# Performance work log

Measured on AMD Instinct MI355X. Metric: run time of the kernel, lower is better.

Reference implementation:

```python
import jax, jax.numpy as jnp
import numpy as np

ITERATION = 10

def setup_inputs() -> dict:
    key = jax.random.key(0)
    k1, k2, k3 = jax.random.split(key, 3)
    a_inter = jax.random.normal(k1, (8, 64, 64, 32, 32), dtype=jnp.float32)
    logits = jax.random.normal(k2, (8, 64), dtype=jnp.float32)
    W = jax.random.normal(k3, (1, 64, 64), dtype=jnp.float32)
    return {"a_inter": a_inter, "logits": logits, "W": W}


def reference(a_inter, logits, W):
    N = W.shape[1]  # num_nodes
    B = a_inter.shape[0]
    # feats: [B, N, C*H*W]
    feats = a_inter[:, :, :N, :, :].reshape(B, N, -1)
    # expand logits [B, N] -> [B, N, N] (unsqueeze(1).expand in torch)
    logits0 = jnp.broadcast_to(logits[:, None, :], (B, N, N))

    feats_norm = jnp.linalg.norm(feats, ord=2, axis=2, keepdims=True)  # [B, N, 1]
    pairwise_norm = feats_norm @ jnp.swapaxes(feats_norm, 1, 2)        # [B, N, N]
    pairwise_dot = feats @ jnp.swapaxes(feats, 1, 2)                   # [B, N, N]
    pairwise_sim = pairwise_dot / (pairwise_norm + 1e-6)
    W_sym = (W + jnp.swapaxes(W, 1, 2)) / 2.0
    pairwise_potential = pairwise_sim * W_sym                          # [B, N, N]

    unary_potential = logits0

    def body(i, l):
        probs = jnp.swapaxes(jax.nn.sigmoid(l), 1, 2)  # [B, N, N]
        # probs*pp - (1-probs)*pp == (2*probs - 1)*pp
        pp_E = jnp.sum((2.0 * probs - 1.0) * pairwise_potential, axis=2, keepdims=True)
        return unary_potential + pp_E

    logits_out = jax.lax.fori_loop(0, ITERATION, body, logits0)
    return logits_out.mean(axis=1)  # [B, N]
```

## Files before the change

kernel.cpp:

```cpp
#include <hip/hip_runtime.h>
#include <math.h>

#define BATCH 8
#define NN 64
#define DD 65536
#define CH 256
#define KC (DD / CH)
#define KSTEPS (KC / 32)

typedef float  floatx4 __attribute__((ext_vector_type(4)));
typedef __bf16 bf16x8  __attribute__((ext_vector_type(8)));

static __device__ __forceinline__ bf16x8 cvt8(float4 lo, float4 hi) {
    const unsigned sel = 0x07060302u;
    union { unsigned u[4]; bf16x8 v; } r;
    r.u[0] = __builtin_amdgcn_perm(__float_as_uint(lo.y), __float_as_uint(lo.x), sel);
    r.u[1] = __builtin_amdgcn_perm(__float_as_uint(lo.w), __float_as_uint(lo.z), sel);
    r.u[2] = __builtin_amdgcn_perm(__float_as_uint(hi.y), __float_as_uint(hi.x), sel);
    r.u[3] = __builtin_amdgcn_perm(__float_as_uint(hi.w), __float_as_uint(hi.z), sel);
    return r.v;
}

__global__ __launch_bounds__(256, 4) void gram_partial_kernel(const float* __restrict__ a,
                                                              float* __restrict__ part) {
    const int bid = blockIdx.x;
    const int b = bid >> 8;
    const int c = bid & (CH - 1);

    const int tid  = threadIdx.x;
    const int w    = tid >> 6;
    const int lane = tid & 63;
    const int m    = lane & 15;
    const int q    = lane >> 4;

    const float* base = a + (size_t)b * NN * DD + (size_t)c * KC
                          + (size_t)m * DD + q * 8;
    const float* p0 = base + (size_t)((w ^ 0) * 16) * DD;
    const float* p1 = base + (size_t)((w ^ 1) * 16) * DD;
    const float* p2 = base + (size_t)((w ^ 2) * 16) * DD;
    const float* p3 = base + (size_t)((w ^ 3) * 16) * DD;

    floatx4 acc[4];
    #pragma unroll
    for (int i = 0; i < 4; ++i) acc[i] = (floatx4)0.0f;

    float4 A0, A1, A2, A3, A4, A5, A6, A7;
    float4 B0, B1, B2, B3, B4, B5, B6, B7;

#define LOADSET(R0,R1,R2,R3,R4,R5,R6,R7, o)                      \
    R0 = *(const float4*)(p0 + (o));  R1 = *(const float4*)(p0 + (o) + 4); \
    R2 = *(const float4*)(p1 + (o));  R3 = *(const float4*)(p1 + (o) + 4); \
    R4 = *(const float4*)(p2 + (o));  R5 = *(const float4*)(p2 + (o) + 4); \
    R6 = *(const float4*)(p3 + (o));  R7 = *(const float4*)(p3 + (o) + 4);

#define MFMASET(R0,R1,R2,R3,R4,R5,R6,R7)                         \
    {                                                            \
        bf16x8 f0 = cvt8(R0, R1);                                \
        bf16x8 f1 = cvt8(R2, R3);                                \
        bf16x8 f2 = cvt8(R4, R5);                                \
        bf16x8 f3 = cvt8(R6, R7);                                \
        acc[0] = __builtin_amdgcn_mfma_f32_16x16x32_bf16(f0, f0, acc[0], 0, 0, 0); \
        acc[1] = __builtin_amdgcn_mfma_f32_16x16x32_bf16(f0, f1, acc[1], 0, 0, 0); \
        acc[2] = __builtin_amdgcn_mfma_f32_16x16x32_bf16(f0, f2, acc[2], 0, 0, 0); \
        acc[3] = __builtin_amdgcn_mfma_f32_16x16x32_bf16(f0, f3, acc[3], 0, 0, 0); \
    }

    LOADSET(A0,A1,A2,A3,A4,A5,A6,A7, 0)
    #pragma unroll
    for (int s = 0; s < KSTEPS; s += 2) {
        if (s + 1 < KSTEPS) { LOADSET(B0,B1,B2,B3,B4,B5,B6,B7, (s + 1) * 32) }
        MFMASET(A0,A1,A2,A3,A4,A5,A6,A7)
        if (s + 2 < KSTEPS) { LOADSET(A0,A1,A2,A3,A4,A5,A6,A7, (s + 2) * 32) }
        if (s + 1 < KSTEPS) { MFMASET(B0,B1,B2,B3,B4,B5,B6,B7) }
    }
#undef LOADSET
#undef MFMASET

    float* pg = part + (size_t)bid * (NN * NN);
    #pragma unroll
    for (int i = 0; i < 4; ++i) {
        const int t = w ^ i;
        float* tp = pg + (w * 4 + t) * 256 + m;
        #pragma unroll
        for (int r = 0; r < 4; ++r)
            tp[(q * 4 + r) * 16] = acc[i][r];
    }
}

__global__ __launch_bounds__(128) void gram_reduce_kernel(const float* __restrict__ part,
                                                          float* __restrict__ gram) {
    const int gid = blockIdx.x * 128 + threadIdx.x;
    const int b   = gid >> 12;
    const int idx = gid & 4095;
    const int i   = idx >> 6;
    const int j   = idx & 63;
    const int off = ((i >> 4) * 4 + (j >> 4)) * 256 + (i & 15) * 16 + (j & 15);
    const float* p = part + (size_t)b * CH * (NN * NN) + off;

    float s0 = 0.f, s1 = 0.f, s2 = 0.f, s3 = 0.f;
    #pragma unroll 4
    for (int c = 0; c < CH; c += 4) {
        s0 += p[(size_t)(c + 0) * (NN * NN)];
        s1 += p[(size_t)(c + 1) * (NN * NN)];
        s2 += p[(size_t)(c + 2) * (NN * NN)];
        s3 += p[(size_t)(c + 3) * (NN * NN)];
    }
    gram[gid] = (s0 + s1) + (s2 + s3);
}

__global__ __launch_bounds__(256) void crf_kernel(const float* __restrict__ gram,
                                                  const float* __restrict__ logits,
                                                  const float* __restrict__ Wm,
                                                  float* __restrict__ out) {
    __shared__ float pp[NN][NN + 1];
    __shared__ float E[NN];
    __shared__ float nrm[NN];
    __shared__ float part[4 * NN];

    const int b  = blockIdx.x;
    const int tid = threadIdx.x;
    const int i  = tid & 63;
    const int jq = tid >> 6;
    const float* g = gram + b * NN * NN;

    if (jq == 0) nrm[i] = sqrtf(g[i * NN + i]);
    E[i] = 0.0f;
    __syncthreads();

    const float ni = nrm[i];
    for (int jj = 0; jj < 16; ++jj) {
        int j = jq * 16 + jj;
        float wsym = 0.5f * (Wm[i * NN + j] + Wm[j * NN + i]);
        pp[i][j] = g[i * NN + j] / (ni * nrm[j] + 1e-6f) * wsym;
    }
    const float li = logits[b * NN + i];
    __syncthreads();

    for (int it = 0; it < 10; ++it) {
        float acc = 0.0f;
        for (int jj = 0; jj < 16; ++jj) {
            int j = jq * 16 + jj;
            float t = li + E[j];
            float s = 1.0f / (1.0f + expf(-t));
            acc = fmaf(2.0f * s - 1.0f, pp[i][j], acc);
        }
        part[jq * NN + i] = acc;
        __syncthreads();
        if (jq == 0)
            E[i] = part[i] + part[NN + i] + part[2 * NN + i] + part[3 * NN + i];
        __syncthreads();
    }

    if (tid < 64) {
        float s = E[tid];
        for (int off = 32; off > 0; off >>= 1) s += __shfl_down(s, off);
        float meanE = __shfl(s, 0) * (1.0f / 64.0f);
        out[b * NN + tid] = logits[b * NN + tid] + meanE;
    }
}

extern "C" void kernel_launch(void* const* d_in, const int* in_sizes, int n_in,
                              void* d_out, int out_size, void* d_ws, size_t ws_size,
                              hipStream_t stream) {
    const float* a      = (const float*)d_in[0];
    const float* logits = (const float*)d_in[1];
    const float* Wm     = (const float*)d_in[2];
    float* out  = (float*)d_out;

    float* part = (float*)d_ws;
    float* gram = part + (size_t)BATCH * CH * NN * NN;

    gram_partial_kernel<<<BATCH * CH, 256, 0, stream>>>(a, part);
    gram_reduce_kernel<<<(BATCH * NN * NN) / 128, 128, 0, stream>>>(part, gram);
    crf_kernel<<<BATCH, 256, 0, stream>>>(gram, logits, Wm, out);
}
```

Before: 251.8 us.

## Split K across waves with full 64x64 Gram per wave and LDS reduction

Each wave now computes the full 64x64 Gram tile over its own K quarter, instead of each wave computing a 16-row stripe over a shared K range. The four wave partials are summed through shared memory inside the block. The grid shrinks from 2048 to 512 blocks, so there are 4x fewer partial tiles to write and reduce. In exchange each wave holds 16 accumulator tiles, which raises register pressure and lowers occupancy. The launch bound of 4 blocks per CU is also dropped.

```diff
diff --git a/kernel.cpp b/kernel.cpp
--- a/kernel.cpp
+++ b/kernel.cpp
@@ -4,9 +4,11 @@
 #define BATCH 8
 #define NN 64
 #define DD 65536
-#define CH 256
-#define KC (DD / CH)
-#define KSTEPS (KC / 32)
+#define BPB 64
+#define NBLK (BATCH * BPB)
+#define KC (DD / BPB)
+#define KW (KC / 4)
+#define KSTEPS (KW / 32)
 
 typedef float  floatx4 __attribute__((ext_vector_type(4)));
 typedef __bf16 bf16x8  __attribute__((ext_vector_type(8)));
@@ -21,11 +23,13 @@
     return r.v;
 }
 
-__global__ __launch_bounds__(256, 4) void gram_partial_kernel(const float* __restrict__ a,
-                                                              float* __restrict__ part) {
+__global__ __launch_bounds__(256) void gram_partial_kernel(const float* __restrict__ a,
+                                                           float* __restrict__ part) {
+    __shared__ __align__(16) float red[3][16][64][4];
+
     const int bid = blockIdx.x;
-    const int b = bid >> 8;
-    const int c = bid & (CH - 1);
+    const int b = bid >> 6;
+    const int c = bid & (BPB - 1);
 
     const int tid  = threadIdx.x;
     const int w    = tid >> 6;
@@ -33,57 +37,83 @@
     const int m    = lane & 15;
     const int q    = lane >> 4;
 
-    const float* base = a + (size_t)b * NN * DD + (size_t)c * KC
+    const float* base = a + (size_t)b * NN * DD + (size_t)c * KC + (size_t)w * KW
                           + (size_t)m * DD + q * 8;
-    const float* p0 = base + (size_t)((w ^ 0) * 16) * DD;
-    const float* p1 = base + (size_t)((w ^ 1) * 16) * DD;
-    const float* p2 = base + (size_t)((w ^ 2) * 16) * DD;
-    const float* p3 = base + (size_t)((w ^ 3) * 16) * DD;
-
-    floatx4 acc[4];
+    const float* p0 = base;
+    const float* p1 = base + (size_t)16 * DD;
+    const float* p2 = base + (size_t)32 * DD;
+    const float* p3 = base + (size_t)48 * DD;
+
+    floatx4 acc[16];
     #pragma unroll
-    for (int i = 0; i < 4; ++i) acc[i] = (floatx4)0.0f;
+    for (int i = 0; i < 16; ++i) acc[i] = (floatx4)0.0f;
 
     float4 A0, A1, A2, A3, A4, A5, A6, A7;
     float4 B0, B1, B2, B3, B4, B5, B6, B7;
 
-#define LOADSET(R0,R1,R2,R3,R4,R5,R6,R7, o)                      \
+#define LOADSET(R0,R1,R2,R3,R4,R5,R6,R7, o)                                \
     R0 = *(const float4*)(p0 + (o));  R1 = *(const float4*)(p0 + (o) + 4); \
     R2 = *(const float4*)(p1 + (o));  R3 = *(const float4*)(p1 + (o) + 4); \
     R4 = *(const float4*)(p2 + (o));  R5 = *(const float4*)(p2 + (o) + 4); \
     R6 = *(const float4*)(p3 + (o));  R7 = *(const float4*)(p3 + (o) + 4);
 
-#define MFMASET(R0,R1,R2,R3,R4,R5,R6,R7)                         \
-    {                                                            \
-        bf16x8 f0 = cvt8(R0, R1);                                \
-        bf16x8 f1 = cvt8(R2, R3);                                \
-        bf16x8 f2 = cvt8(R4, R5);                                \
-        bf16x8 f3 = cvt8(R6, R7);                                \
-        acc[0] = __builtin_amdgcn_mfma_f32_16x16x32_bf16(f0, f0, acc[0], 0, 0, 0); \
-        acc[1] = __builtin_amdgcn_mfma_f32_16x16x32_bf16(f0, f1, acc[1], 0, 0, 0); \
-        acc[2] = __builtin_amdgcn_mfma_f32_16x16x32_bf16(f0, f2, acc[2], 0, 0, 0); \
-        acc[3] = __builtin_amdgcn_mfma_f32_16x16x32_bf16(f0, f3, acc[3], 0, 0, 0); \
+#define MFMASET(R0,R1,R2,R3,R4,R5,R6,R7)                                   \
+    {                                                                      \
+        bf16x8 f0 = cvt8(R0, R1);                                          \
+        bf16x8 f1 = cvt8(R2, R3);                                          \
+        bf16x8 f2 = cvt8(R4, R5);                                          \
+        bf16x8 f3 = cvt8(R6, R7);                                          \
+        acc[ 0] = __builtin_amdgcn_mfma_f32_16x16x32_bf16(f0, f0, acc[ 0], 0, 0, 0); \
+        acc[ 1] = __builtin_amdgcn_mfma_f32_16x16x32_bf16(f0, f1, acc[ 1], 0, 0, 0); \
+        acc[ 2] = __builtin_amdgcn_mfma_f32_16x16x32_bf16(f0, f2, acc[ 2], 0, 0, 0); \
+        acc[ 3] = __builtin_amdgcn_mfma_f32_16x16x32_bf16(f0, f3, acc[ 3], 0, 0, 0); \
+        acc[ 4] = __builtin_amdgcn_mfma_f32_16x16x32_bf16(f1, f0, acc[ 4], 0, 0, 0); \
+        acc[ 5] = __builtin_amdgcn_mfma_f32_16x16x32_bf16(f1, f1, acc[ 5], 0, 0, 0); \
+        acc[ 6] = __builtin_amdgcn_mfma_f32_16x16x32_bf16(f1, f2, acc[ 6], 0, 0, 0); \
+        acc[ 7] = __builtin_amdgcn_mfma_f32_16x16x32_bf16(f1, f3, acc[ 7], 0, 0, 0); \
+        acc[ 8] = __builtin_amdgcn_mfma_f32_16x16x32_bf16(f2, f0, acc[ 8], 0, 0, 0); \
+        acc[ 9] = __builtin_amdgcn_mfma_f32_16x16x32_bf16(f2, f1, acc[ 9], 0, 0, 0); \
+        acc[10] = __builtin_amdgcn_mfma_f32_16x16x32_bf16(f2, f2, acc[10], 0, 0, 0); \
+        acc[11] = __builtin_amdgcn_mfma_f32_16x16x32_bf16(f2, f3, acc[11], 0, 0, 0); \
+        acc[12] = __builtin_amdgcn_mfma_f32_16x16x32_bf16(f3, f0, acc[12], 0, 0, 0); \
+        acc[13] = __builtin_amdgcn_mfma_f32_16x16x32_bf16(f3, f1, acc[13], 0, 0, 0); \
+        acc[14] = __builtin_amdgcn_mfma_f32_16x16x32_bf16(f3, f2, acc[14], 0, 0, 0); \
+        acc[15] = __builtin_amdgcn_mfma_f32_16x16x32_bf16(f3, f3, acc[15], 0, 0, 0); \
     }
 
     LOADSET(A0,A1,A2,A3,A4,A5,A6,A7, 0)
     #pragma unroll
     for (int s = 0; s < KSTEPS; s += 2) {
-        if (s + 1 < KSTEPS) { LOADSET(B0,B1,B2,B3,B4,B5,B6,B7, (s + 1) * 32) }
+        LOADSET(B0,B1,B2,B3,B4,B5,B6,B7, (s + 1) * 32)
         MFMASET(A0,A1,A2,A3,A4,A5,A6,A7)
         if (s + 2 < KSTEPS) { LOADSET(A0,A1,A2,A3,A4,A5,A6,A7, (s + 2) * 32) }
-        if (s + 1 < KSTEPS) { MFMASET(B0,B1,B2,B3,B4,B5,B6,B7) }
+        MFMASET(B0,B1,B2,B3,B4,B5,B6,B7)
     }
 #undef LOADSET
 #undef MFMASET
 
-    float* pg = part + (size_t)bid * (NN * NN);
-    #pragma unroll
-    for (int i = 0; i < 4; ++i) {
-        const int t = w ^ i;
-        float* tp = pg + (w * 4 + t) * 256 + m;
+    if (w > 0) {
         #pragma unroll
-        for (int r = 0; r < 4; ++r)
-            tp[(q * 4 + r) * 16] = acc[i][r];
+        for (int t = 0; t < 16; ++t)
+            *(floatx4*)&red[w - 1][t][lane][0] = acc[t];
+    }
+    __syncthreads();
+    if (w == 0) {
+        #pragma unroll
+        for (int t = 0; t < 16; ++t) {
+            floatx4 r0 = *(const floatx4*)&red[0][t][lane][0];
+            floatx4 r1 = *(const floatx4*)&red[1][t][lane][0];
+            floatx4 r2 = *(const floatx4*)&red[2][t][lane][0];
+            acc[t] += (r0 + r1) + r2;
+        }
+        float* pg = part + (size_t)bid * (NN * NN);
+        #pragma unroll
+        for (int t = 0; t < 16; ++t) {
+            float* tp = pg + t * 256 + m;
+            #pragma unroll
+            for (int r = 0; r < 4; ++r)
+                tp[(q * 4 + r) * 16] = acc[t][r];
+        }
     }
 }
 
@@ -95,11 +125,11 @@
     const int i   = idx >> 6;
     const int j   = idx & 63;
     const int off = ((i >> 4) * 4 + (j >> 4)) * 256 + (i & 15) * 16 + (j & 15);
-    const float* p = part + (size_t)b * CH * (NN * NN) + off;
+    const float* p = part + (size_t)b * BPB * (NN * NN) + off;
 
     float s0 = 0.f, s1 = 0.f, s2 = 0.f, s3 = 0.f;
     #pragma unroll 4
-    for (int c = 0; c < CH; c += 4) {
+    for (int c = 0; c < BPB; c += 4) {
         s0 += p[(size_t)(c + 0) * (NN * NN)];
         s1 += p[(size_t)(c + 1) * (NN * NN)];
         s2 += p[(size_t)(c + 2) * (NN * NN)];
@@ -168,9 +198,9 @@
     float* out  = (float*)d_out;
 
     float* part = (float*)d_ws;
-    float* gram = part + (size_t)BATCH * CH * NN * NN;
-
-    gram_partial_kernel<<<BATCH * CH, 256, 0, stream>>>(a, part);
+    float* gram = part + (size_t)NBLK * NN * NN;
+
+    gram_partial_kernel<<<NBLK, 256, 0, stream>>>(a, part);
     gram_reduce_kernel<<<(BATCH * NN * NN) / 128, 128, 0, stream>>>(part, gram);
     crf_kernel<<<BATCH, 256, 0, stream>>>(gram, logits, Wm, out);
 }
```

New measurement: 224.3 us. 10.9% less time.
